# Performance work log

Measured on AMD Instinct MI355X. Metric: run time of the kernel, lower is better.

Reference implementation:

```python
import jax, jax.numpy as jnp
import numpy as np

QMAX = 127.0

def _sym_quantize(t):
    # per-tensor symmetric int8 fake-quant: returns (quantized values as float, scale)
    scale = jnp.max(jnp.abs(t)) / QMAX
    q = jnp.clip(jnp.round(t / scale), -QMAX, QMAX)
    return q, scale

def setup_inputs() -> dict:
    key = jax.random.key(0)
    k1, k2, k3 = jax.random.split(key, 3)
    TOKENS, IN_F, OUT_F = 4096, 4096, 4096
    x = jax.random.normal(k1, (TOKENS, IN_F), dtype=jnp.float32)
    # int8-valued weight buffer (stored int32 for portability), symmetric range
    quantized_weight = jax.random.randint(k2, (OUT_F, IN_F), -127, 128, dtype=jnp.int32)
    weight_scale = jnp.float32(0.01)  # scalar per-tensor weight scale buffer
    bias = jax.random.normal(k3, (OUT_F,), dtype=jnp.float32)
    return {"x": x, "quantized_weight": quantized_weight,
            "weight_scale": weight_scale, "bias": bias}

def reference(x, quantized_weight, weight_scale, bias):
    q_x, x_scale = _sym_quantize(x)                      # [T, In] fake-quant activations
    w = quantized_weight.astype(jnp.float32)             # [Out, In]
    out = jnp.matmul(q_x, w.T)                           # fp32 GEMM on int8-valued operands
    out = out * (x_scale * weight_scale)                 # dequant scaling
    out = out + bias
    return out
```

## Files before the change

kernel.cpp:

```cpp
#include <hip/hip_runtime.h>

typedef __attribute__((ext_vector_type(4))) int int4v;

#define NB_MAX 1024

__device__ __forceinline__ void async_ld16(const void* g, void* l) {
  __builtin_amdgcn_global_load_lds(
      (const __attribute__((address_space(1))) void*)g,
      (__attribute__((address_space(3))) void*)l,
      16, 0, 0);
}

__global__ void absmax_partial_kernel(const float* __restrict__ x,
                                      float* __restrict__ partial, int n4) {
  const float4* x4 = (const float4*)x;
  float m = 0.0f;
  for (int i = blockIdx.x * blockDim.x + threadIdx.x; i < n4;
       i += gridDim.x * blockDim.x) {
    float4 v = x4[i];
    m = fmaxf(m, fabsf(v.x));
    m = fmaxf(m, fabsf(v.y));
    m = fmaxf(m, fabsf(v.z));
    m = fmaxf(m, fabsf(v.w));
  }
#pragma unroll
  for (int off = 32; off > 0; off >>= 1)
    m = fmaxf(m, __shfl_down(m, off, 64));
  __shared__ float wmax[4];
  const int wid = threadIdx.x >> 6;
  if ((threadIdx.x & 63) == 0) wmax[wid] = m;
  __syncthreads();
  if (threadIdx.x == 0)
    partial[blockIdx.x] =
        fmaxf(fmaxf(wmax[0], wmax[1]), fmaxf(wmax[2], wmax[3]));
}

__device__ __forceinline__ float reduce_partials(const float* partial) {
  __shared__ float smax;
  float m = 0.0f;
  for (int i = threadIdx.x; i < NB_MAX; i += blockDim.x)
    m = fmaxf(m, partial[i]);
#pragma unroll
  for (int off = 32; off > 0; off >>= 1)
    m = fmaxf(m, __shfl_down(m, off, 64));
  __shared__ float wmax[4];
  const int wid = threadIdx.x >> 6;
  if ((threadIdx.x & 63) == 0) wmax[wid] = m;
  __syncthreads();
  if (threadIdx.x == 0)
    smax = fmaxf(fmaxf(wmax[0], wmax[1]), fmaxf(wmax[2], wmax[3]));
  __syncthreads();
  return smax;
}

__global__ void quant_pack_kernel(const float* __restrict__ x,
                                  const int* __restrict__ w,
                                  const float* __restrict__ partial,
                                  float* __restrict__ scale_slot,
                                  int* __restrict__ qx, int* __restrict__ qw,
                                  int nx4, int nw4) {
  const float scale = reduce_partials(partial) / 127.0f;
  const int i = blockIdx.x * blockDim.x + threadIdx.x;
  if (i == 0) *scale_slot = scale;
  if (i < nx4) {
    float4 v = ((const float4*)x)[i];
    int q0 = (int)fminf(fmaxf(rintf(v.x / scale), -127.0f), 127.0f);
    int q1 = (int)fminf(fmaxf(rintf(v.y / scale), -127.0f), 127.0f);
    int q2 = (int)fminf(fmaxf(rintf(v.z / scale), -127.0f), 127.0f);
    int q3 = (int)fminf(fmaxf(rintf(v.w / scale), -127.0f), 127.0f);
    unsigned int p = (unsigned int)(q0 & 255) |
                     ((unsigned int)(q1 & 255) << 8) |
                     ((unsigned int)(q2 & 255) << 16) |
                     ((unsigned int)(q3 & 255) << 24);
    qx[i] = (int)p;
  }
  if (i < nw4) {
    int4 v = ((const int4*)w)[i];
    unsigned int p = (unsigned int)(v.x & 255) |
                     ((unsigned int)(v.y & 255) << 8) |
                     ((unsigned int)(v.z & 255) << 16) |
                     ((unsigned int)(v.w & 255) << 24);
    qw[i] = (int)p;
  }
}

__global__ __launch_bounds__(512, 2) void gemm_i8_kernel(
    const signed char* __restrict__ A,
    const signed char* __restrict__ B,
    const float* __restrict__ bias,
    const float* __restrict__ scale_slot,
    const float* __restrict__ wscale,
    float* __restrict__ out, int K, int N) {
  __shared__ signed char As[2][256 * 128];
  __shared__ signed char Bs[2][256 * 128];

  const int tid = threadIdx.x;
  const int lane = tid & 63;
  const int wid = tid >> 6;

  const int nwgx = gridDim.x;
  const int nwg = nwgx * gridDim.y;
  const int flat = blockIdx.y * nwgx + blockIdx.x;
  const int cpx = nwg >> 3;
  const int swz = (flat & 7) * cpx + (flat >> 3);
  const int row0 = (swz / nwgx) << 8;
  const int col0 = (swz % nwgx) << 8;

  const int wm = (wid >> 2) * 128;
  const int wn = (wid & 3) * 64;

  int4v acc[8][4] = {};

  const int srow = wid * 8 + (lane >> 3);
  const int schunk = ((lane & 7) ^ ((lane >> 3) & 7)) << 4;
  const signed char* gA = A + (long)(row0 + srow) * K + schunk;
  const signed char* gB = B + (long)(col0 + srow) * K + schunk;
  const int sdst = wid * 1024;

  const int q = lane >> 4;
  const int c7 = lane & 7;
  const int fc0 = (q ^ c7) << 4;
  const int fc1 = ((4 + q) ^ c7) << 4;
  const int fa = (wm + (lane & 15)) * 128;
  const int fb = (wn + (lane & 15)) * 128;

  const long l64K = 64 * (long)K;
  const int NT = K >> 7;

  async_ld16(gB, &Bs[0][0 * 8192 + sdst]);
  async_ld16(gB + l64K, &Bs[0][1 * 8192 + sdst]);
  async_ld16(gB + 2 * l64K, &Bs[0][2 * 8192 + sdst]);
  async_ld16(gB + 3 * l64K, &Bs[0][3 * 8192 + sdst]);
  async_ld16(gA, &As[0][0 * 8192 + sdst]);
  async_ld16(gA + 2 * l64K, &As[0][2 * 8192 + sdst]);
  async_ld16(gA + l64K, &As[0][1 * 8192 + sdst]);
  async_ld16(gA + 3 * l64K, &As[0][3 * 8192 + sdst]);
  asm volatile("s_waitcnt vmcnt(2)" ::: "memory");
  __builtin_amdgcn_s_barrier();

  int4v areg[4][2], breg0[2][2], breg1[2][2];

  for (int T = 0; T < NT; ++T) {
    const int b = T & 1;
    const int Tn = (T + 1 < NT) ? (T + 1) : T;
    const signed char* gAn = gA + (long)Tn * 128;
    const signed char* gBn = gB + (long)Tn * 128;
    signed char* An = &As[b ^ 1][sdst];
    signed char* Bn = &Bs[b ^ 1][sdst];
    const signed char* Ab = As[b];
    const signed char* Bb = Bs[b];

#pragma unroll
    for (int i = 0; i < 4; i++) {
      areg[i][0] = *(const int4v*)(Ab + fa + i * 2048 + fc0);
      areg[i][1] = *(const int4v*)(Ab + fa + i * 2048 + fc1);
    }
#pragma unroll
    for (int j = 0; j < 2; j++) {
      breg0[j][0] = *(const int4v*)(Bb + fb + j * 2048 + fc0);
      breg0[j][1] = *(const int4v*)(Bb + fb + j * 2048 + fc1);
    }
    async_ld16(gBn, Bn);
    async_ld16(gBn + l64K, Bn + 8192);
    __builtin_amdgcn_s_barrier();
    asm volatile("s_waitcnt lgkmcnt(0)" ::: "memory");
    __builtin_amdgcn_s_setprio(1);
#pragma unroll
    for (int i = 0; i < 4; i++)
#pragma unroll
      for (int j = 0; j < 2; j++) {
        acc[i][j] = __builtin_amdgcn_mfma_i32_16x16x64_i8(areg[i][0], breg0[j][0], acc[i][j], 0, 0, 0);
        acc[i][j] = __builtin_amdgcn_mfma_i32_16x16x64_i8(areg[i][1], breg0[j][1], acc[i][j], 0, 0, 0);
      }
    __builtin_amdgcn_s_setprio(0);
    __builtin_amdgcn_s_barrier();

#pragma unroll
    for (int j = 0; j < 2; j++) {
      breg1[j][0] = *(const int4v*)(Bb + fb + (2 + j) * 2048 + fc0);
      breg1[j][1] = *(const int4v*)(Bb + fb + (2 + j) * 2048 + fc1);
    }
    async_ld16(gBn + 2 * l64K, Bn + 2 * 8192);
    async_ld16(gBn + 3 * l64K, Bn + 3 * 8192);
    __builtin_amdgcn_s_barrier();
    asm volatile("s_waitcnt lgkmcnt(0)" ::: "memory");
    __builtin_amdgcn_s_setprio(1);
#pragma unroll
    for (int i = 0; i < 4; i++)
#pragma unroll
      for (int j = 0; j < 2; j++) {
        acc[i][2 + j] = __builtin_amdgcn_mfma_i32_16x16x64_i8(areg[i][0], breg1[j][0], acc[i][2 + j], 0, 0, 0);
        acc[i][2 + j] = __builtin_amdgcn_mfma_i32_16x16x64_i8(areg[i][1], breg1[j][1], acc[i][2 + j], 0, 0, 0);
      }
    __builtin_amdgcn_s_setprio(0);
    asm volatile("s_waitcnt vmcnt(4)" ::: "memory");
    __builtin_amdgcn_s_barrier();

#pragma unroll
    for (int i = 0; i < 4; i++) {
      areg[i][0] = *(const int4v*)(Ab + fa + 8192 + i * 2048 + fc0);
      areg[i][1] = *(const int4v*)(Ab + fa + 8192 + i * 2048 + fc1);
    }
    async_ld16(gAn, An);
    async_ld16(gAn + 2 * l64K, An + 2 * 8192);
    __builtin_amdgcn_s_barrier();
    asm volatile("s_waitcnt lgkmcnt(0)" ::: "memory");
    __builtin_amdgcn_s_setprio(1);
#pragma unroll
    for (int i = 0; i < 4; i++)
#pragma unroll
      for (int j = 0; j < 2; j++) {
        acc[4 + i][j] = __builtin_amdgcn_mfma_i32_16x16x64_i8(areg[i][0], breg0[j][0], acc[4 + i][j], 0, 0, 0);
        acc[4 + i][j] = __builtin_amdgcn_mfma_i32_16x16x64_i8(areg[i][1], breg0[j][1], acc[4 + i][j], 0, 0, 0);
      }
    __builtin_amdgcn_s_setprio(0);
    __builtin_amdgcn_s_barrier();

    async_ld16(gAn + l64K, An + 8192);
    async_ld16(gAn + 3 * l64K, An + 3 * 8192);
    __builtin_amdgcn_s_barrier();
    __builtin_amdgcn_s_setprio(1);
#pragma unroll
    for (int i = 0; i < 4; i++)
#pragma unroll
      for (int j = 0; j < 2; j++) {
        acc[4 + i][2 + j] = __builtin_amdgcn_mfma_i32_16x16x64_i8(areg[i][0], breg1[j][0], acc[4 + i][2 + j], 0, 0, 0);
        acc[4 + i][2 + j] = __builtin_amdgcn_mfma_i32_16x16x64_i8(areg[i][1], breg1[j][1], acc[4 + i][2 + j], 0, 0, 0);
      }
    __builtin_amdgcn_s_setprio(0);
    asm volatile("s_waitcnt vmcnt(2)" ::: "memory");
    __builtin_amdgcn_s_barrier();
  }

  asm volatile("s_waitcnt vmcnt(0)" ::: "memory");

  const float s = scale_slot[0] * wscale[0];
  const int orow = row0 + wm + (q << 2);
  const int ocol = col0 + wn + (lane & 15);
#pragma unroll
  for (int jj = 0; jj < 4; jj++) {
    const int c = ocol + jj * 16;
    const float bv = bias[c];
#pragma unroll
    for (int i = 0; i < 8; i++) {
#pragma unroll
      for (int r = 0; r < 4; r++) {
        out[(long)(orow + i * 16 + r) * N + c] = (float)acc[i][jj][r] * s + bv;
      }
    }
  }
}

extern "C" void kernel_launch(void* const* d_in, const int* in_sizes, int n_in,
                              void* d_out, int out_size, void* d_ws,
                              size_t ws_size, hipStream_t stream) {
  const float* x = (const float*)d_in[0];
  const int* w = (const int*)d_in[1];
  const float* wscale = (const float*)d_in[2];
  const float* bias = (const float*)d_in[3];
  float* out = (float*)d_out;

  const int OUT_F = in_sizes[3];
  const int IN_F = in_sizes[1] / OUT_F;
  const int TOKENS = in_sizes[0] / IN_F;

  float* partial = (float*)d_ws;
  float* scale_slot = partial + NB_MAX;
  signed char* qx = (signed char*)d_ws + 8192;
  signed char* qw = qx + (size_t)TOKENS * IN_F;

  const int nx4 = TOKENS * IN_F / 4;
  const int nw4 = OUT_F * IN_F / 4;

  absmax_partial_kernel<<<NB_MAX, 256, 0, stream>>>(x, partial, nx4);

  const int nmax = nx4 > nw4 ? nx4 : nw4;
  quant_pack_kernel<<<(nmax + 255) / 256, 256, 0, stream>>>(
      x, w, partial, scale_slot, (int*)qx, (int*)qw, nx4, nw4);

  dim3 grid(OUT_F / 256, TOKENS / 256);
  gemm_i8_kernel<<<grid, 512, 0, stream>>>(qx, qw, bias, scale_slot, wscale,
                                           out, IN_F, OUT_F);
}
```

Measured before the change: 245.8 us.

## Move weight packing into absmax pass, restructure GEMM prefetch and stage epilogue via LDS

```diff
diff --git a/kernel.cpp b/kernel.cpp
--- a/kernel.cpp
+++ b/kernel.cpp
@@ -11,17 +11,28 @@
       16, 0, 0);
 }
 
-__global__ void absmax_partial_kernel(const float* __restrict__ x,
-                                      float* __restrict__ partial, int n4) {
+__global__ void absmax_wpack_kernel(const float* __restrict__ x,
+                                    const int* __restrict__ w,
+                                    float* __restrict__ partial,
+                                    int* __restrict__ qw, int n4, int nw4) {
   const float4* x4 = (const float4*)x;
   float m = 0.0f;
-  for (int i = blockIdx.x * blockDim.x + threadIdx.x; i < n4;
-       i += gridDim.x * blockDim.x) {
+  const int stride = gridDim.x * blockDim.x;
+  const int i0 = blockIdx.x * blockDim.x + threadIdx.x;
+  for (int i = i0; i < n4; i += stride) {
     float4 v = x4[i];
     m = fmaxf(m, fabsf(v.x));
     m = fmaxf(m, fabsf(v.y));
     m = fmaxf(m, fabsf(v.z));
     m = fmaxf(m, fabsf(v.w));
+  }
+  for (int i = i0; i < nw4; i += stride) {
+    int4 v = ((const int4*)w)[i];
+    unsigned int p = (unsigned int)(v.x & 255) |
+                     ((unsigned int)(v.y & 255) << 8) |
+                     ((unsigned int)(v.z & 255) << 16) |
+                     ((unsigned int)(v.w & 255) << 24);
+    qw[i] = (int)p;
   }
 #pragma unroll
   for (int off = 32; off > 0; off >>= 1)
@@ -53,16 +64,14 @@
   return smax;
 }
 
-__global__ void quant_pack_kernel(const float* __restrict__ x,
-                                  const int* __restrict__ w,
-                                  const float* __restrict__ partial,
-                                  float* __restrict__ scale_slot,
-                                  int* __restrict__ qx, int* __restrict__ qw,
-                                  int nx4, int nw4) {
+__global__ void quant_x_kernel(const float* __restrict__ x,
+                               const float* __restrict__ partial,
+                               float* __restrict__ scale_slot,
+                               int* __restrict__ qx, int nx4) {
   const float scale = reduce_partials(partial) / 127.0f;
-  const int i = blockIdx.x * blockDim.x + threadIdx.x;
-  if (i == 0) *scale_slot = scale;
-  if (i < nx4) {
+  if (blockIdx.x == 0 && threadIdx.x == 0) *scale_slot = scale;
+  const int stride = gridDim.x * blockDim.x;
+  for (int i = blockIdx.x * blockDim.x + threadIdx.x; i < nx4; i += stride) {
     float4 v = ((const float4*)x)[i];
     int q0 = (int)fminf(fmaxf(rintf(v.x / scale), -127.0f), 127.0f);
     int q1 = (int)fminf(fmaxf(rintf(v.y / scale), -127.0f), 127.0f);
@@ -74,14 +83,6 @@
                      ((unsigned int)(q3 & 255) << 24);
     qx[i] = (int)p;
   }
-  if (i < nw4) {
-    int4 v = ((const int4*)w)[i];
-    unsigned int p = (unsigned int)(v.x & 255) |
-                     ((unsigned int)(v.y & 255) << 8) |
-                     ((unsigned int)(v.z & 255) << 16) |
-                     ((unsigned int)(v.w & 255) << 24);
-    qw[i] = (int)p;
-  }
 }
 
 __global__ __launch_bounds__(512, 2) void gemm_i8_kernel(
@@ -142,9 +143,9 @@
 
   for (int T = 0; T < NT; ++T) {
     const int b = T & 1;
-    const int Tn = (T + 1 < NT) ? (T + 1) : T;
-    const signed char* gAn = gA + (long)Tn * 128;
-    const signed char* gBn = gB + (long)Tn * 128;
+    const bool pf = (T + 1 < NT);
+    const signed char* gAn = gA + (long)(T + 1) * 128;
+    const signed char* gBn = gB + (long)(T + 1) * 128;
     signed char* An = &As[b ^ 1][sdst];
     signed char* Bn = &Bs[b ^ 1][sdst];
     const signed char* Ab = As[b];
@@ -160,8 +161,12 @@
       breg0[j][0] = *(const int4v*)(Bb + fb + j * 2048 + fc0);
       breg0[j][1] = *(const int4v*)(Bb + fb + j * 2048 + fc1);
     }
-    async_ld16(gBn, Bn);
-    async_ld16(gBn + l64K, Bn + 8192);
+    if (pf) {
+      async_ld16(gBn, Bn);
+      async_ld16(gBn + l64K, Bn + 8192);
+      async_ld16(gBn + 2 * l64K, Bn + 2 * 8192);
+      async_ld16(gBn + 3 * l64K, Bn + 3 * 8192);
+    }
     __builtin_amdgcn_s_barrier();
     asm volatile("s_waitcnt lgkmcnt(0)" ::: "memory");
     __builtin_amdgcn_s_setprio(1);
@@ -180,8 +185,12 @@
       breg1[j][0] = *(const int4v*)(Bb + fb + (2 + j) * 2048 + fc0);
       breg1[j][1] = *(const int4v*)(Bb + fb + (2 + j) * 2048 + fc1);
     }
-    async_ld16(gBn + 2 * l64K, Bn + 2 * 8192);
-    async_ld16(gBn + 3 * l64K, Bn + 3 * 8192);
+    if (pf) {
+      async_ld16(gAn, An);
+      async_ld16(gAn + 2 * l64K, An + 2 * 8192);
+      async_ld16(gAn + l64K, An + 8192);
+      async_ld16(gAn + 3 * l64K, An + 3 * 8192);
+    }
     __builtin_amdgcn_s_barrier();
     asm volatile("s_waitcnt lgkmcnt(0)" ::: "memory");
     __builtin_amdgcn_s_setprio(1);
@@ -193,7 +202,11 @@
         acc[i][2 + j] = __builtin_amdgcn_mfma_i32_16x16x64_i8(areg[i][1], breg1[j][1], acc[i][2 + j], 0, 0, 0);
       }
     __builtin_amdgcn_s_setprio(0);
-    asm volatile("s_waitcnt vmcnt(4)" ::: "memory");
+    if (pf) {
+      asm volatile("s_waitcnt vmcnt(8)" ::: "memory");
+    } else {
+      asm volatile("s_waitcnt vmcnt(0)" ::: "memory");
+    }
     __builtin_amdgcn_s_barrier();
 
 #pragma unroll
@@ -201,8 +214,6 @@
       areg[i][0] = *(const int4v*)(Ab + fa + 8192 + i * 2048 + fc0);
       areg[i][1] = *(const int4v*)(Ab + fa + 8192 + i * 2048 + fc1);
     }
-    async_ld16(gAn, An);
-    async_ld16(gAn + 2 * l64K, An + 2 * 8192);
     __builtin_amdgcn_s_barrier();
     asm volatile("s_waitcnt lgkmcnt(0)" ::: "memory");
     __builtin_amdgcn_s_setprio(1);
@@ -216,8 +227,6 @@
     __builtin_amdgcn_s_setprio(0);
     __builtin_amdgcn_s_barrier();
 
-    async_ld16(gAn + l64K, An + 8192);
-    async_ld16(gAn + 3 * l64K, An + 3 * 8192);
     __builtin_amdgcn_s_barrier();
     __builtin_amdgcn_s_setprio(1);
 #pragma unroll
@@ -233,20 +242,31 @@
   }
 
   asm volatile("s_waitcnt vmcnt(0)" ::: "memory");
-
+  __syncthreads();
+
+  float* lds = (float*)&As[0][0];
   const float s = scale_slot[0] * wscale[0];
-  const int orow = row0 + wm + (q << 2);
-  const int ocol = col0 + wn + (lane & 15);
-#pragma unroll
-  for (int jj = 0; jj < 4; jj++) {
-    const int c = ocol + jj * 16;
-    const float bv = bias[c];
-#pragma unroll
-    for (int i = 0; i < 8; i++) {
-#pragma unroll
-      for (int r = 0; r < 4; r++) {
-        out[(long)(orow + i * 16 + r) * N + c] = (float)acc[i][jj][r] * s + bv;
-      }
+  const int l15 = lane & 15;
+  float bv[4];
+#pragma unroll
+  for (int jj = 0; jj < 4; jj++) bv[jj] = bias[col0 + wn + l15 + jj * 16];
+  const int wbase = wid << 11;
+#pragma unroll
+  for (int g = 0; g < 8; ++g) {
+    float* reg = lds + wbase + ((g & 1) << 10);
+#pragma unroll
+    for (int jj = 0; jj < 4; jj++)
+#pragma unroll
+      for (int r = 0; r < 4; r++)
+        reg[(q * 4 + r) * 64 + l15 + jj * 16] = (float)acc[g][jj][r] * s + bv[jj];
+    asm volatile("s_waitcnt lgkmcnt(0)" ::: "memory");
+    __builtin_amdgcn_sched_barrier(0);
+#pragma unroll
+    for (int rr = 0; rr < 4; rr++) {
+      const int row = q + rr * 4;
+      float4 v = *(const float4*)(reg + row * 64 + l15 * 4);
+      *(float4*)(out + (long)(row0 + wm + g * 16 + row) * N + col0 + wn +
+                 l15 * 4) = v;
     }
   }
 }
@@ -272,11 +292,11 @@
   const int nx4 = TOKENS * IN_F / 4;
   const int nw4 = OUT_F * IN_F / 4;
 
-  absmax_partial_kernel<<<NB_MAX, 256, 0, stream>>>(x, partial, nx4);
-
-  const int nmax = nx4 > nw4 ? nx4 : nw4;
-  quant_pack_kernel<<<(nmax + 255) / 256, 256, 0, stream>>>(
-      x, w, partial, scale_slot, (int*)qx, (int*)qw, nx4, nw4);
+  absmax_wpack_kernel<<<NB_MAX, 256, 0, stream>>>(x, w, partial, (int*)qw,
+                                                  nx4, nw4);
+
+  quant_x_kernel<<<2048, 256, 0, stream>>>(x, partial, scale_slot, (int*)qx,
+                                           nx4);
 
   dim3 grid(OUT_F / 256, TOKENS / 256);
   gemm_i8_kernel<<<grid, 512, 0, stream>>>(qx, qw, bias, scale_slot, wscale,
```

Measured after the change: 244.6 us. No clear change (-0.5%).
